# Kernel tuning notes

Hardware: AMD Instinct MI355X
Metric: run time of the kernel (lower is better)

The kernel has to match this reference:

```python
import jax, jax.numpy as jnp
import numpy as np

# Dims: B batch, CK key dim, CV value dim, NOBJ objects, T memory frames, HxW feature map
B, CK, CV, NOBJ, T, H, W = 1, 64, 512, 2, 2, 64, 64


def setup_inputs() -> dict:
    key = jax.random.key(0)
    k1, k2, k3, k4, k5 = jax.random.split(key, 5)
    return {
        "query_key": jax.random.normal(k1, (B, CK, H, W), jnp.float32),
        "query_selection": jax.random.uniform(k2, (B, CK, H, W), jnp.float32),
        "memory_key": jax.random.normal(k3, (B, CK, T, H, W), jnp.float32),
        "memory_shrinkage": jax.random.uniform(k4, (B, 1, T, H, W), jnp.float32),
        "memory_value": jax.random.normal(k5, (B, NOBJ, CV, T, H, W), jnp.float32),
    }


def reference(query_key, query_selection, memory_key, memory_shrinkage, memory_value):
    b, nobj, cv = memory_value.shape[:3]
    ck = memory_key.shape[1]
    h, w = query_key.shape[-2:]
    hw = h * w
    mk = memory_key.reshape(b, ck, -1)            # (b, ck, N) with N = T*H*W
    ms = memory_shrinkage.reshape(b, -1)          # (b, N)
    qk = query_key.reshape(b, ck, hw)             # (b, ck, hw)
    qe = query_selection.reshape(b, ck, hw)       # (b, ck, hw)
    mv = memory_value.reshape(b, nobj * cv, -1)   # (b, nobj*cv, N)

    # Negative L2 similarity with selection weighting (XMem get_similarity)
    a_sq = jnp.einsum('bcn,bcp->bnp', mk * mk, qe)            # (b, N, hw)
    two_ab = 2.0 * jnp.einsum('bcn,bcp->bnp', mk, qk * qe)    # (b, N, hw)
    b_sq = jnp.sum(qe * qk * qk, axis=1, keepdims=True)       # (b, 1, hw)
    inv_sqrt_ck = np.float32(1.0 / np.sqrt(ck))
    sim = (two_ab - a_sq - b_sq) * ms[:, :, None] * inv_sqrt_ck

    # Softmax over memory slots (dim N), then weighted readout
    aff = jax.nn.softmax(sim, axis=1)                          # (b, N, hw)
    mem = jnp.einsum('bvn,bnp->bvp', mv, aff)                  # (b, nobj*cv, hw)
    return mem.reshape(b, nobj, cv, h, w)
```

## Files before the change

kernel.cpp:

```cpp
#include <hip/hip_runtime.h>
#include <stdint.h>

typedef unsigned short u16;
typedef __attribute__((ext_vector_type(4))) float f32x4;
typedef __attribute__((ext_vector_type(8))) __bf16 bf16x8;
typedef __attribute__((ext_vector_type(4))) unsigned int u32x4;

#define HWPX 4096
#define NMEM 8192
#define CKD  64
#define VROWS 1024

__device__ __forceinline__ u16 f2bf(float x) {
    union { float f; unsigned u; } v; v.f = x;
    unsigned r = v.u + 0x7FFFu + ((v.u >> 16) & 1u);
    return (u16)(r >> 16);
}

__device__ __forceinline__ void gld_lds16(const void* g, void* l) {
    __builtin_amdgcn_global_load_lds(
        (const __attribute__((address_space(1))) uint32_t*)g,
        (__attribute__((address_space(3))) uint32_t*)l, 16, 0, 0);
}

__global__ void prep_all(const float* __restrict__ qk, const float* __restrict__ qe,
                         const float* __restrict__ mk, const float* __restrict__ mv,
                         u16* __restrict__ Qhat, float* __restrict__ bsq,
                         u16* __restrict__ Khat, u16* __restrict__ mvb,
                         float* __restrict__ denom) {
    const int bx = blockIdx.x;
    const int tid = threadIdx.x;
    if (bx < 16) {
        int p = bx * 256 + tid;
        float acc = 0.f;
        #pragma unroll 4
        for (int c = 0; c < CKD; ++c) {
            float k = qk[c * HWPX + p];
            float e = qe[c * HWPX + p];
            Qhat[p * 128 + c]      = f2bf(k * e);
            Qhat[p * 128 + 64 + c] = f2bf(e);
            acc += e * k * k;
        }
        bsq[p] = acc;
        denom[p] = 0.f;
    } else if (bx < 48) {
        int n = (bx - 16) * 256 + tid;
        #pragma unroll 4
        for (int c = 0; c < CKD; ++c) {
            float m = mk[c * NMEM + n];
            Khat[n * 128 + c]      = f2bf(2.f * m);
            Khat[n * 128 + 64 + c] = f2bf(-m * m);
        }
    } else {
        int i = (bx - 48) * 256 + tid;
        float4 v = ((const float4*)mv)[i];
        u16 o0 = f2bf(v.x), o1 = f2bf(v.y), o2 = f2bf(v.z), o3 = f2bf(v.w);
        unsigned lo = (unsigned)o0 | ((unsigned)o1 << 16);
        unsigned hi = (unsigned)o2 | ((unsigned)o3 << 16);
        ((uint2*)mvb)[i] = make_uint2(lo, hi);
    }
}

__launch_bounds__(256)
__global__ void gemm1_kernel(const u16* __restrict__ Qhat, const u16* __restrict__ Khat,
                             const float* __restrict__ bsq, const float* __restrict__ ms,
                             u16* __restrict__ Pt, float* __restrict__ denom) {
    __shared__ __align__(16) u16 smem[32768];
    u16* Qs = smem;
    u16* Ks = smem + 16384;

    const int tid  = threadIdx.x;
    const int l    = tid & 63;
    const int w    = tid >> 6;
    const int quad = l >> 4;
    const int l15  = l & 15;
    const int wm = w >> 1, wn = w & 1;
    const int p0 = blockIdx.x * 128;
    const int n0 = blockIdx.y * 128;

    {
        const int rsub = tid >> 4;
        const int csw  = (tid & 15) ^ (rsub & 15);
        #pragma unroll
        for (int rnd = 0; rnd < 8; ++rnd) {
            gld_lds16(Qhat + (size_t)(p0 + rnd * 16 + rsub) * 128 + csw * 8,
                      Qs + rnd * 2048 + w * 512);
            gld_lds16(Khat + (size_t)(n0 + rnd * 16 + rsub) * 128 + csw * 8,
                      Ks + rnd * 2048 + w * 512);
        }
    }
    __syncthreads();

    f32x4 acc[4][4] = {};
    #pragma unroll
    for (int kk = 0; kk < 4; ++kk) {
        bf16x8 a[4], b[4];
        #pragma unroll
        for (int mi = 0; mi < 4; ++mi) {
            int row = wm * 64 + mi * 16 + l15;
            a[mi] = *(const bf16x8*)(Qs + row * 128 + (((kk * 4 + quad) ^ l15) << 3));
        }
        #pragma unroll
        for (int ni = 0; ni < 4; ++ni) {
            int row = wn * 64 + ni * 16 + l15;
            b[ni] = *(const bf16x8*)(Ks + row * 128 + (((kk * 4 + quad) ^ l15) << 3));
        }
        #pragma unroll
        for (int mi = 0; mi < 4; ++mi)
            #pragma unroll
            for (int ni = 0; ni < 4; ++ni)
                acc[mi][ni] = __builtin_amdgcn_mfma_f32_16x16x32_bf16(a[mi], b[ni], acc[mi][ni], 0, 0, 0);
    }

    float msv[4];
    #pragma unroll
    for (int ni = 0; ni < 4; ++ni)
        msv[ni] = ms[n0 + wn * 64 + ni * 16 + l15] * 0.125f;
    float bsv[4][4];
    #pragma unroll
    for (int mi = 0; mi < 4; ++mi)
        #pragma unroll
        for (int r = 0; r < 4; ++r)
            bsv[mi][r] = bsq[p0 + wm * 64 + mi * 16 + quad * 4 + r];

    __syncthreads();
    u16* Ps = smem;
    float rowsum[4][4] = {};
    #pragma unroll
    for (int mi = 0; mi < 4; ++mi) {
        #pragma unroll
        for (int ni = 0; ni < 4; ++ni) {
            f32x4 v = acc[mi][ni];
            int col = wn * 64 + ni * 16 + l15;
            #pragma unroll
            for (int r = 0; r < 4; ++r) {
                int rowl = wm * 64 + mi * 16 + quad * 4 + r;
                float pv = __expf((v[r] - bsv[mi][r]) * msv[ni]);
                rowsum[mi][r] += pv;
                Ps[rowl * 136 + col] = f2bf(pv);
            }
        }
    }
    #pragma unroll
    for (int mi = 0; mi < 4; ++mi)
        #pragma unroll
        for (int r = 0; r < 4; ++r) {
            float s = rowsum[mi][r];
            s += __shfl_xor(s, 1);
            s += __shfl_xor(s, 2);
            s += __shfl_xor(s, 4);
            s += __shfl_xor(s, 8);
            rowsum[mi][r] = s;
        }
    {
        float myv = 0.f;
        #pragma unroll
        for (int mi = 0; mi < 4; ++mi)
            #pragma unroll
            for (int r = 0; r < 4; ++r)
                if (l15 == mi * 4 + r) myv = rowsum[mi][r];
        atomicAdd(&denom[p0 + wm * 64 + (l15 >> 2) * 16 + quad * 4 + (l15 & 3)], myv);
    }
    __syncthreads();

    {
        const size_t tileOff = ((size_t)blockIdx.x * 64 + blockIdx.y) * 16384;
        int row = tid >> 1, half = tid & 1;
        const u32x4* src = (const u32x4*)(Ps + row * 136 + half * 64);
        u32x4* dst = (u32x4*)(Pt + tileOff + row * 128 + half * 64);
        #pragma unroll
        for (int i = 0; i < 8; ++i) dst[i] = src[i];
    }
}

__launch_bounds__(256, 4)
__global__ void gemm2_kernel(const u16* __restrict__ Ab, const u16* __restrict__ Bt,
                             float* __restrict__ outacc) {
    __shared__ __align__(16) u16 As[128 * 64];
    __shared__ __align__(16) u16 Bs[128 * 64];

    const int tid  = threadIdx.x;
    const int l    = tid & 63;
    const int w    = tid >> 6;
    const int quad = l >> 4;
    const int l15  = l & 15;
    const int wm = w >> 1, wn = w & 1;

    const int lin = blockIdx.x + (blockIdx.y << 3) + (blockIdx.z << 8);
    const int vb  = (lin >> 3) & 7;
    const int pb  = (lin & 7) | (((lin >> 6) & 3) << 3);
    const int kz  = lin >> 8;
    const int v0 = vb * 128;
    const int p0 = pb * 128;
    const int kbeg = kz * (NMEM / 4);
    const int kend = kbeg + (NMEM / 4);

    const int rsub = tid >> 3;
    const int csw  = (tid & 7) ^ (rsub & 7);

    f32x4 acc[4][4] = {};

    for (int k0 = kbeg; k0 < kend; k0 += 64) {
        const int nb = k0 >> 7;
        const int nh = (k0 >> 6) & 1;
        const u16* bsrc = Bt + ((size_t)pb * 64 + nb) * 16384 + nh * 64;
        __syncthreads();
        #pragma unroll
        for (int rnd = 0; rnd < 4; ++rnd) {
            gld_lds16(Ab + (size_t)(v0 + rnd * 32 + rsub) * NMEM + k0 + csw * 8,
                      As + rnd * 2048 + w * 512);
            gld_lds16(bsrc + (rnd * 32 + rsub) * 128 + csw * 8,
                      Bs + rnd * 2048 + w * 512);
        }
        __syncthreads();
        #pragma unroll
        for (int kk = 0; kk < 2; ++kk) {
            bf16x8 a[4], b[4];
            #pragma unroll
            for (int mi = 0; mi < 4; ++mi) {
                int row = wm * 64 + mi * 16 + l15;
                a[mi] = *(const bf16x8*)(As + row * 64 + (((kk * 4 + quad) ^ (l15 & 7)) << 3));
            }
            #pragma unroll
            for (int ni = 0; ni < 4; ++ni) {
                int row = wn * 64 + ni * 16 + l15;
                b[ni] = *(const bf16x8*)(Bs + row * 64 + (((kk * 4 + quad) ^ (l15 & 7)) << 3));
            }
            #pragma unroll
            for (int mi = 0; mi < 4; ++mi)
                #pragma unroll
                for (int ni = 0; ni < 4; ++ni)
                    acc[mi][ni] = __builtin_amdgcn_mfma_f32_16x16x32_bf16(a[mi], b[ni], acc[mi][ni], 0, 0, 0);
        }
    }

    #pragma unroll
    for (int mi = 0; mi < 4; ++mi) {
        #pragma unroll
        for (int ni = 0; ni < 4; ++ni) {
            int col = p0 + wn * 64 + ni * 16 + l15;
            f32x4 v = acc[mi][ni];
            #pragma unroll
            for (int r = 0; r < 4; ++r) {
                int row = v0 + wm * 64 + mi * 16 + quad * 4 + r;
                atomicAdd(&outacc[(size_t)row * HWPX + col], v[r]);
            }
        }
    }
}

__global__ void divide_out(float* __restrict__ out, const float* __restrict__ denom) {
    int f = blockIdx.x * 256 + threadIdx.x;
    float4 v = ((float4*)out)[f];
    int p4 = f & (HWPX / 4 - 1);
    float4 d = ((const float4*)denom)[p4];
    v.x /= d.x; v.y /= d.y; v.z /= d.z; v.w /= d.w;
    ((float4*)out)[f] = v;
}

extern "C" void kernel_launch(void* const* d_in, const int* in_sizes, int n_in,
                              void* d_out, int out_size, void* d_ws, size_t ws_size,
                              hipStream_t stream) {
    const float* qk = (const float*)d_in[0];
    const float* qe = (const float*)d_in[1];
    const float* mk = (const float*)d_in[2];
    const float* ms = (const float*)d_in[3];
    const float* mv = (const float*)d_in[4];
    float* out = (float*)d_out;

    char* ws = (char*)d_ws;
    u16*   Pt    = (u16*)ws;
    u16*   mvb   = (u16*)(ws + ((size_t)64 << 20));
    u16*   Khat  = (u16*)(ws + ((size_t)80 << 20));
    u16*   Qhat  = (u16*)(ws + ((size_t)82 << 20));
    float* bsq   = (float*)(ws + ((size_t)83 << 20));
    float* denom = (float*)(ws + ((size_t)83 << 20) + 65536);

    hipMemsetAsync(out, 0, (size_t)VROWS * HWPX * sizeof(float), stream);
    prep_all<<<48 + 8192, 256, 0, stream>>>(qk, qe, mk, mv, Qhat, bsq, Khat, mvb, denom);

    dim3 g1(HWPX / 128, NMEM / 128);
    gemm1_kernel<<<g1, 256, 0, stream>>>(Qhat, Khat, bsq, ms, Pt, denom);

    dim3 g2(8, 32, 4);
    gemm2_kernel<<<g2, 256, 0, stream>>>(mvb, Pt, out);

    divide_out<<<(VROWS * HWPX / 4) / 256, 256, 0, stream>>>(out, denom);
}
```

Measured before the change: 249.2 us.

## Fuse output zeroing into prep, fold normalization into gemm2, halve gemm1 LDS

The memset of the output moves into the prep kernel as extra blocks, and the separate divide pass is removed by scaling each partial sum by the reciprocal denominator before the atomic add in gemm2. gemm1 now loads K in two 64-wide halves, which cuts its shared memory so it can fit under a 4-blocks-per-CU launch bound. The aim is to drop one full read-modify-write pass over the 16MB output and one launch, and to raise gemm1 occupancy, at the cost of an extra sync in gemm1.

Result: faster. 233.0 us (-6.5%).

```diff
diff --git a/kernel.cpp b/kernel.cpp
--- a/kernel.cpp
+++ b/kernel.cpp
@@ -27,7 +27,7 @@
                          const float* __restrict__ mk, const float* __restrict__ mv,
                          u16* __restrict__ Qhat, float* __restrict__ bsq,
                          u16* __restrict__ Khat, u16* __restrict__ mvb,
-                         float* __restrict__ denom) {
+                         float* __restrict__ denom, float* __restrict__ outz) {
     const int bx = blockIdx.x;
     const int tid = threadIdx.x;
     if (bx < 16) {
@@ -51,23 +51,26 @@
             Khat[n * 128 + c]      = f2bf(2.f * m);
             Khat[n * 128 + 64 + c] = f2bf(-m * m);
         }
-    } else {
+    } else if (bx < 48 + 8192) {
         int i = (bx - 48) * 256 + tid;
         float4 v = ((const float4*)mv)[i];
         u16 o0 = f2bf(v.x), o1 = f2bf(v.y), o2 = f2bf(v.z), o3 = f2bf(v.w);
         unsigned lo = (unsigned)o0 | ((unsigned)o1 << 16);
         unsigned hi = (unsigned)o2 | ((unsigned)o3 << 16);
         ((uint2*)mvb)[i] = make_uint2(lo, hi);
-    }
-}
-
-__launch_bounds__(256)
+    } else {
+        int i = (bx - 48 - 8192) * 256 + tid;
+        ((float4*)outz)[i] = make_float4(0.f, 0.f, 0.f, 0.f);
+    }
+}
+
+__launch_bounds__(256, 4)
 __global__ void gemm1_kernel(const u16* __restrict__ Qhat, const u16* __restrict__ Khat,
                              const float* __restrict__ bsq, const float* __restrict__ ms,
                              u16* __restrict__ Pt, float* __restrict__ denom) {
-    __shared__ __align__(16) u16 smem[32768];
+    __shared__ __align__(16) u16 smem[17408];
     u16* Qs = smem;
-    u16* Ks = smem + 16384;
+    u16* Ks = smem + 8192;
 
     const int tid  = threadIdx.x;
     const int l    = tid & 63;
@@ -78,38 +81,41 @@
     const int p0 = blockIdx.x * 128;
     const int n0 = blockIdx.y * 128;
 
-    {
-        const int rsub = tid >> 4;
-        const int csw  = (tid & 15) ^ (rsub & 15);
-        #pragma unroll
-        for (int rnd = 0; rnd < 8; ++rnd) {
-            gld_lds16(Qhat + (size_t)(p0 + rnd * 16 + rsub) * 128 + csw * 8,
+    const int rsub = tid >> 3;
+    const int csw  = (tid & 7) ^ (rsub & 7);
+
+    f32x4 acc[4][4] = {};
+
+    #pragma unroll
+    for (int h = 0; h < 2; ++h) {
+        if (h) __syncthreads();
+        #pragma unroll
+        for (int rnd = 0; rnd < 4; ++rnd) {
+            gld_lds16(Qhat + (size_t)(p0 + rnd * 32 + rsub) * 128 + h * 64 + csw * 8,
                       Qs + rnd * 2048 + w * 512);
-            gld_lds16(Khat + (size_t)(n0 + rnd * 16 + rsub) * 128 + csw * 8,
+            gld_lds16(Khat + (size_t)(n0 + rnd * 32 + rsub) * 128 + h * 64 + csw * 8,
                       Ks + rnd * 2048 + w * 512);
         }
-    }
-    __syncthreads();
-
-    f32x4 acc[4][4] = {};
-    #pragma unroll
-    for (int kk = 0; kk < 4; ++kk) {
-        bf16x8 a[4], b[4];
-        #pragma unroll
-        for (int mi = 0; mi < 4; ++mi) {
-            int row = wm * 64 + mi * 16 + l15;
-            a[mi] = *(const bf16x8*)(Qs + row * 128 + (((kk * 4 + quad) ^ l15) << 3));
-        }
-        #pragma unroll
-        for (int ni = 0; ni < 4; ++ni) {
-            int row = wn * 64 + ni * 16 + l15;
-            b[ni] = *(const bf16x8*)(Ks + row * 128 + (((kk * 4 + quad) ^ l15) << 3));
-        }
-        #pragma unroll
-        for (int mi = 0; mi < 4; ++mi)
-            #pragma unroll
-            for (int ni = 0; ni < 4; ++ni)
-                acc[mi][ni] = __builtin_amdgcn_mfma_f32_16x16x32_bf16(a[mi], b[ni], acc[mi][ni], 0, 0, 0);
+        __syncthreads();
+        #pragma unroll
+        for (int kk = 0; kk < 2; ++kk) {
+            bf16x8 a[4], b[4];
+            #pragma unroll
+            for (int mi = 0; mi < 4; ++mi) {
+                int row = wm * 64 + mi * 16 + l15;
+                a[mi] = *(const bf16x8*)(Qs + row * 64 + (((kk * 4 + quad) ^ (l15 & 7)) << 3));
+            }
+            #pragma unroll
+            for (int ni = 0; ni < 4; ++ni) {
+                int row = wn * 64 + ni * 16 + l15;
+                b[ni] = *(const bf16x8*)(Ks + row * 64 + (((kk * 4 + quad) ^ (l15 & 7)) << 3));
+            }
+            #pragma unroll
+            for (int mi = 0; mi < 4; ++mi)
+                #pragma unroll
+                for (int ni = 0; ni < 4; ++ni)
+                    acc[mi][ni] = __builtin_amdgcn_mfma_f32_16x16x32_bf16(a[mi], b[ni], acc[mi][ni], 0, 0, 0);
+        }
     }
 
     float msv[4];
@@ -175,7 +181,7 @@
 
 __launch_bounds__(256, 4)
 __global__ void gemm2_kernel(const u16* __restrict__ Ab, const u16* __restrict__ Bt,
-                             float* __restrict__ outacc) {
+                             const float* __restrict__ denom, float* __restrict__ outacc) {
     __shared__ __align__(16) u16 As[128 * 64];
     __shared__ __align__(16) u16 Bs[128 * 64];
 
@@ -234,6 +240,11 @@
         }
     }
 
+    float dinv[4];
+    #pragma unroll
+    for (int ni = 0; ni < 4; ++ni)
+        dinv[ni] = 1.0f / denom[p0 + wn * 64 + ni * 16 + l15];
+
     #pragma unroll
     for (int mi = 0; mi < 4; ++mi) {
         #pragma unroll
@@ -243,19 +254,10 @@
             #pragma unroll
             for (int r = 0; r < 4; ++r) {
                 int row = v0 + wm * 64 + mi * 16 + quad * 4 + r;
-                atomicAdd(&outacc[(size_t)row * HWPX + col], v[r]);
-            }
-        }
-    }
-}
-
-__global__ void divide_out(float* __restrict__ out, const float* __restrict__ denom) {
-    int f = blockIdx.x * 256 + threadIdx.x;
-    float4 v = ((float4*)out)[f];
-    int p4 = f & (HWPX / 4 - 1);
-    float4 d = ((const float4*)denom)[p4];
-    v.x /= d.x; v.y /= d.y; v.z /= d.z; v.w /= d.w;
-    ((float4*)out)[f] = v;
+                atomicAdd(&outacc[(size_t)row * HWPX + col], v[r] * dinv[ni]);
+            }
+        }
+    }
 }
 
 extern "C" void kernel_launch(void* const* d_in, const int* in_sizes, int n_in,
@@ -276,14 +278,12 @@
     float* bsq   = (float*)(ws + ((size_t)83 << 20));
     float* denom = (float*)(ws + ((size_t)83 << 20) + 65536);
 
-    hipMemsetAsync(out, 0, (size_t)VROWS * HWPX * sizeof(float), stream);
-    prep_all<<<48 + 8192, 256, 0, stream>>>(qk, qe, mk, mv, Qhat, bsq, Khat, mvb, denom);
+    prep_all<<<48 + 8192 + 4096, 256, 0, stream>>>(qk, qe, mk, mv, Qhat, bsq, Khat, mvb,
+                                                   denom, out);
 
     dim3 g1(HWPX / 128, NMEM / 128);
     gemm1_kernel<<<g1, 256, 0, stream>>>(Qhat, Khat, bsq, ms, Pt, denom);
 
     dim3 g2(8, 32, 4);
-    gemm2_kernel<<<g2, 256, 0, stream>>>(mvb, Pt, out);
-
-    divide_out<<<(VROWS * HWPX / 4) / 256, 256, 0, stream>>>(out, denom);
-}
+    gemm2_kernel<<<g2, 256, 0, stream>>>(mvb, Pt, denom, out);
+}
```
